# Kernel optimization log

Hardware: AMD Instinct MI355X
Metric: run time of the kernel (lower is better)

Reference implementation:

```python
import jax, jax.numpy as jnp
import numpy as np

A = 100000          # num atoms
E = 1600000         # num edges
N_SPECIES = 4       # len(atomic_types)
N_RADIAL = 8        # l=1 radial functions (max_radial hyper)
N_PSEUDO = 4        # Alchemical pseudo species
D = N_RADIAL * N_PSEUDO  # embedding_dim = 32
RC = 5.0            # cutoff radius
WIDTH = 0.5         # shifted-cosine width


def setup_inputs() -> dict:
    key = jax.random.key(0)
    ks = jax.random.split(key, 9)
    return {
        "interatomic_vectors": jax.random.normal(ks[0], (E, 3), dtype=jnp.float32),
        "centers": jax.random.randint(ks[1], (E,), 0, A),
        "neighbors": jax.random.randint(ks[2], (E,), 0, A),
        "species": jax.random.randint(ks[3], (A,), 0, N_SPECIES),
        "structures": jnp.sort(jax.random.randint(ks[4], (A,), 0, 64)),
        "atom_index_in_structure": jax.random.randint(ks[5], (A,), 0, A),
        # learned params
        "W_alch": jax.random.normal(ks[6], (N_SPECIES, N_PSEUDO), dtype=jnp.float32) * 0.1,
        "center_embedding": jax.random.normal(ks[7], (N_SPECIES, D), dtype=jnp.float32),
        "W_contract": jax.random.normal(ks[8], (3, D), dtype=jnp.float32) * (1.0 / np.sqrt(D)),
    }


def _shifted_cosine(d):
    # 1 below rc-width, smooth cosine taper to 0 at rc
    inner = RC - WIDTH
    taper = 0.5 * (jnp.cos(jnp.pi * (d - inner) / WIDTH) + 1.0)
    return jnp.where(d < inner, 1.0, jnp.where(d < RC, taper, 0.0))


def reference(interatomic_vectors, centers, neighbors, species, structures,
              atom_index_in_structure, W_alch, center_embedding, W_contract):
    eps = 1e-12
    d = jnp.sqrt(jnp.sum(interatomic_vectors * interatomic_vectors, axis=1) + eps)  # (E,)
    fc = _shifted_cosine(d)                                                         # (E,)
    # Laplacian-eigenstate-style l=1 radial basis: sin(n*pi*d/rc)/d, n=1..N_RADIAL
    n = jnp.arange(1, N_RADIAL + 1, dtype=jnp.float32)
    R = jnp.sin(n[None, :] * (jnp.pi / RC) * d[:, None]) / d[:, None]               # (E, nR)
    # real l=1 spherical harmonics, m order (-1, 0, 1) -> (y, z, x)/d
    Y = interatomic_vectors[:, jnp.array([1, 2, 0])] / d[:, None]                   # (E, 3)
    # alchemical pseudo-species weights of the neighbor
    alch = W_alch[species[neighbors]]                                               # (E, nQ)
    # per-edge expansion coefficients, scattered onto centers
    edge = (fc[:, None, None, None]
            * Y[:, :, None, None]
            * R[:, None, :, None]
            * alch[:, None, None, :])                                               # (E, 3, nR, nQ)
    spex = jax.ops.segment_sum(edge, centers, num_segments=A)                       # (A, 3, nR, nQ)
    x = spex.reshape(A, 3, D)                                                       # reshape(n,q -> n*q)
    x = x * center_embedding[species][:, None, :]                                   # center encoding
    out = jnp.einsum("amd,od->amo", x, W_contract)                                  # (A, 3, 3)
    return out
```

## Files before the change

kernel.cpp:

```cpp
#include <hip/hip_runtime.h>
#include <hip/hip_fp16.h>


constexpr int NSP  = 4;
constexpr int NRAD = 8;
constexpr int NPS  = 4;
constexpr int DDIM = NRAD * NPS;

constexpr int APB       = 128;
constexpr int APB_SH    = 7;
constexpr int NBIN_PAD  = 832;
constexpr int NROWS_PAD = 832;
constexpr int RS        = 840;
constexpr int PH1_BLK   = 512;
constexpr int PH1_U     = 4;
constexpr int PH1_REC   = PH1_BLK * PH1_U;
constexpr int CAP2      = 1536;
constexpr int IT2       = CAP2 / 256;

__device__ __forceinline__ unsigned pack2(float a, float b) {
    union { __half2 h; unsigned u; } cv;
    cv.h = __floats2half2_rn(a, b);
    return cv.u;
}
__device__ __forceinline__ float2 unpack2(unsigned u) {
    union { unsigned u; __half2 h; } cv;
    cv.u = u;
    return __half22float2(cv.h);
}

__device__ __forceinline__ void build_w2(
    float* sW2, const float* cemb, const float* Wc, const float* W_alch,
    int tid, int nthreads)
{
    for (int i = tid; i < 3 * NRAD * 16; i += nthreads) {
        int p  = i & 15;
        int n  = (i >> 4) & 7;
        int o  = i >> 7;
        int sc = p >> 2, sn = p & 3;
        float w = 0.0f;
        #pragma unroll
        for (int q = 0; q < NPS; q++)
            w += cemb[sc * DDIM + n * NPS + q] * Wc[o * DDIM + n * NPS + q]
               * W_alch[sn * NPS + q];
        sW2[i] = w;
    }
}

__device__ __forceinline__ bool edge_math(
    float vx, float vy, float vz, int pair, const float* sW2,
    float g[3], float t[3])
{
    float d2    = vx * vx + vy * vy + vz * vz + 1e-12f;
    float d     = sqrtf(d2);
    float inv_d = 1.0f / d;

    const float PI = 3.14159265358979323846f;
    const float RCUT = 5.0f, INNER = 4.5f, INVW = 2.0f;
    if (d >= RCUT) return false;
    float taper = 0.5f * (cosf(PI * (d - INNER) * INVW) + 1.0f);
    float fc = (d < INNER) ? 1.0f : taper;

    float theta = (PI / RCUT) * d;
    float s1 = sinf(theta);
    float c1 = cosf(theta);
    float two_c = 2.0f * c1;
    float R[NRAD];
    R[0] = s1 * inv_d;
    float sm2 = 0.0f, sm1 = s1;
    #pragma unroll
    for (int n = 1; n < NRAD; n++) {
        float s = two_c * sm1 - sm2;
        sm2 = sm1; sm1 = s;
        R[n] = s * inv_d;
    }

    #pragma unroll
    for (int o = 0; o < 3; o++) {
        float acc = 0.0f;
        #pragma unroll
        for (int n = 0; n < NRAD; n++)
            acc += R[n] * sW2[(o * NRAD + n) * 16 + pair];
        t[o] = acc;
    }
    g[0] = fc * vy * inv_d;
    g[1] = fc * vz * inv_d;
    g[2] = fc * vx * inv_d;
    return true;
}

__global__ __launch_bounds__(PH1_BLK) void vb_phase1(
    const float* __restrict__ vecs,
    const int*   __restrict__ centers,
    const int*   __restrict__ neighbors,
    const int*   __restrict__ species,
    const float* __restrict__ W_alch,
    const float* __restrict__ cemb,
    const float* __restrict__ Wc,
    unsigned short* __restrict__ runoff,
    int4*        __restrict__ payload,
    int E, int nbin)
{
    __shared__ float sW2[3 * NRAD * 16];
    __shared__ int4  srec[PH1_REC];
    __shared__ unsigned lcntP[NBIN_PAD / 2];
    __shared__ unsigned short lexcl[NBIN_PAD];
    __shared__ int sTotal;

    int tid = threadIdx.x;
    build_w2(sW2, cemb, Wc, W_alch, tid, PH1_BLK);
    for (int i = tid; i < NBIN_PAD / 2; i += PH1_BLK) lcntP[i] = 0;
    __syncthreads();

    int4 rec[PH1_U];
    int  rnk[PH1_U];
    #pragma unroll
    for (int u = 0; u < PH1_U; u++) {
        int e = blockIdx.x * PH1_REC + u * PH1_BLK + tid;
        rec[u].x = -1;
        rnk[u]   = 0;
        if (e < E) {
            float vx = vecs[3 * e + 0];
            float vy = vecs[3 * e + 1];
            float vz = vecs[3 * e + 2];
            int c  = centers[e];
            int pair = species[c] * 4 + species[neighbors[e]];
            float g[3], t[3];
            if (edge_math(vx, vy, vz, pair, sW2, g, t)) {
                rec[u].x = c;
                rec[u].y = (int)pack2(g[0], g[1]);
                rec[u].z = (int)pack2(g[2], t[0]);
                rec[u].w = (int)pack2(t[1], t[2]);
                int bin = c >> APB_SH;
                int sh  = (bin & 1) << 4;
                unsigned old = atomicAdd(&lcntP[bin >> 1], 1u << sh);
                rnk[u] = (int)((old >> sh) & 0xffff);
            }
        }
    }
    __syncthreads();

    if (tid < 64) {
        int base = tid * 13;
        int pre[13];
        int sum = 0;
        #pragma unroll
        for (int j = 0; j < 13; j++) {
            int b = base + j;
            int n = (lcntP[b >> 1] >> ((b & 1) << 4)) & 0xffff;
            pre[j] = sum; sum += n;
        }
        int incl = sum;
        #pragma unroll
        for (int off = 1; off < 64; off <<= 1) {
            int t = __shfl_up(incl, off, 64);
            if (tid >= off) incl += t;
        }
        int ex = incl - sum;
        #pragma unroll
        for (int j = 0; j < 13; j++)
            lexcl[base + j] = (unsigned short)(ex + pre[j]);
        if (tid == 63) sTotal = incl;
    }
    __syncthreads();

    #pragma unroll
    for (int u = 0; u < PH1_U; u++) {
        if (rec[u].x >= 0) {
            int bin = rec[u].x >> APB_SH;
            srec[(int)lexcl[bin] + rnk[u]] = rec[u];
        }
    }
    __syncthreads();

    int total = sTotal;
    size_t pbase = (size_t)blockIdx.x * PH1_REC;
    for (int i = tid; i < total; i += PH1_BLK)
        payload[pbase + i] = srec[i];
    unsigned short* ro = runoff + (size_t)blockIdx.x * RS;
    for (int b = tid; b <= nbin; b += PH1_BLK)
        ro[b] = (b < nbin) ? lexcl[b] : (unsigned short)total;
}

__global__ __launch_bounds__(256) void vb_phase2(
    const unsigned short* __restrict__ runoff,
    const int4*           __restrict__ payload,
    float*                __restrict__ out,
    int A, int nblocks)
{
    __shared__ int4 srec2[CAP2];
    __shared__ unsigned short sidx[CAP2];
    __shared__ unsigned short sst[NROWS_PAD];
    __shared__ unsigned short roff[NROWS_PAD + 64];
    __shared__ int cnt[APB], aexcl[APB];
    __shared__ float sout[APB * 9];
    __shared__ int sTotal;

    int b   = blockIdx.x;
    int tid = threadIdx.x;

    for (int r = tid; r < NROWS_PAD; r += 256) {
        unsigned short s0 = 0, len = 0;
        if (r < nblocks) {
            const unsigned short* row = runoff + (size_t)r * RS + b;
            s0  = row[0];
            len = (unsigned short)(row[1] - row[0]);
        }
        sst[r]  = s0;
        roff[r] = len;
    }
    __syncthreads();

    if (tid < 64) {
        int base = tid * 13;
        int pre[13];
        int sum = 0;
        #pragma unroll
        for (int j = 0; j < 13; j++) { pre[j] = sum; sum += roff[base + j]; }
        int incl = sum;
        #pragma unroll
        for (int off = 1; off < 64; off <<= 1) {
            int t = __shfl_up(incl, off, 64);
            if (tid >= off) incl += t;
        }
        int ex = incl - sum;
        #pragma unroll
        for (int j = 0; j < 13; j++)
            roff[base + j] = (unsigned short)(ex + pre[j]);
        if (tid == 63) sTotal = incl;
    }
    __syncthreads();
    if (tid == 0) roff[NROWS_PAD] = (unsigned short)sTotal;
    __syncthreads();

    int total = sTotal;
    float acc[9] = {0,0,0,0,0,0,0,0,0};
    int half = tid >> 7;
    int atom = tid & (APB - 1);

    for (int w0 = 0; w0 < total; w0 += CAP2) {
        int wend = min(w0 + CAP2, total);
        int nc = wend - w0;

        if (tid < APB) cnt[tid] = 0;
        __syncthreads();

        int key6[IT2], rnk6[IT2];
        #pragma unroll
        for (int it = 0; it < IT2; it++) {
            int i = it * 256 + tid;
            key6[it] = -1;
            rnk6[it] = 0;
            if (i < nc) {
                int p = w0 + i;
                int l = 0, h = nblocks;
                #pragma unroll 1
                while (h - l > 1) {
                    int m = (l + h) >> 1;
                    if ((int)roff[m] <= p) l = m; else h = m;
                }
                int j = p - (int)roff[l];
                int4 r = payload[(size_t)l * PH1_REC + (int)sst[l] + j];
                srec2[i] = r;
                int k = r.x & (APB - 1);
                key6[it] = k;
                rnk6[it] = atomicAdd(&cnt[k], 1);
            }
        }
        __syncthreads();

        if (tid < 64) {
            int c0 = cnt[2 * tid], c1 = cnt[2 * tid + 1];
            int s1 = c0 + c1;
            int incl = s1;
            #pragma unroll
            for (int off = 1; off < 64; off <<= 1) {
                int t = __shfl_up(incl, off, 64);
                if (tid >= off) incl += t;
            }
            int ex = incl - s1;
            aexcl[2 * tid]     = ex;
            aexcl[2 * tid + 1] = ex + c0;
        }
        __syncthreads();

        #pragma unroll
        for (int it = 0; it < IT2; it++) {
            if (key6[it] >= 0)
                sidx[aexcl[key6[it]] + rnk6[it]] =
                    (unsigned short)(it * 256 + tid);
        }
        __syncthreads();

        {
            int st = aexcl[atom], n = cnt[atom];
            int mid = st + ((n + 1) >> 1);
            int lo = half ? mid : st;
            int hi = half ? (st + n) : mid;
            for (int j = lo; j < hi; j++) {
                int4 r = srec2[sidx[j]];
                float2 g01 = unpack2((unsigned)r.y);
                float2 g2t = unpack2((unsigned)r.z);
                float2 t12 = unpack2((unsigned)r.w);
                float g0 = g01.x, g1 = g01.y, g2 = g2t.x;
                float t0 = g2t.y, t1 = t12.x, t2 = t12.y;
                acc[0] += g0 * t0; acc[1] += g0 * t1; acc[2] += g0 * t2;
                acc[3] += g1 * t0; acc[4] += g1 * t1; acc[5] += g1 * t2;
                acc[6] += g2 * t0; acc[7] += g2 * t1; acc[8] += g2 * t2;
            }
        }
        __syncthreads();
    }

    if (half == 0) {
        #pragma unroll
        for (int k = 0; k < 9; k++) sout[atom * 9 + k] = acc[k];
    }
    __syncthreads();
    if (half == 1) {
        #pragma unroll
        for (int k = 0; k < 9; k++) sout[atom * 9 + k] += acc[k];
    }
    __syncthreads();
    size_t gbase = (size_t)b * APB * 9;
    size_t lim = (size_t)A * 9;
    for (int i = tid; i < APB * 9; i += 256) {
        size_t gi = gbase + i;
        if (gi < lim) out[gi] = sout[i];
    }
}

__global__ __launch_bounds__(256) void vb_edge_fallback(
    const float* __restrict__ vecs,
    const int*   __restrict__ centers,
    const int*   __restrict__ neighbors,
    const int*   __restrict__ species,
    const float* __restrict__ W_alch,
    const float* __restrict__ cemb,
    const float* __restrict__ Wc,
    float*       __restrict__ out,
    int E)
{
    __shared__ float sW2[3 * NRAD * 16];
    build_w2(sW2, cemb, Wc, W_alch, threadIdx.x, blockDim.x);
    __syncthreads();

    int e = blockIdx.x * blockDim.x + threadIdx.x;
    if (e >= E) return;
    float vx = vecs[3 * e + 0], vy = vecs[3 * e + 1], vz = vecs[3 * e + 2];
    int c = centers[e];
    int pair = species[c] * 4 + species[neighbors[e]];
    float g[3], t[3];
    if (!edge_math(vx, vy, vz, pair, sW2, g, t)) return;
    float* op = out + (size_t)c * 9;
    #pragma unroll
    for (int m = 0; m < 3; m++)
        #pragma unroll
        for (int o = 0; o < 3; o++)
            atomicAdd(op + m * 3 + o, g[m] * t[o]);
}

extern "C" void kernel_launch(void* const* d_in, const int* in_sizes, int n_in,
                              void* d_out, int out_size, void* d_ws, size_t ws_size,
                              hipStream_t stream) {
    const float* vecs      = (const float*)d_in[0];
    const int*   centers   = (const int*)d_in[1];
    const int*   neighbors = (const int*)d_in[2];
    const int*   species   = (const int*)d_in[3];
    const float* W_alch    = (const float*)d_in[6];
    const float* cemb      = (const float*)d_in[7];
    const float* Wc        = (const float*)d_in[8];
    float*       out       = (float*)d_out;

    int E = in_sizes[1];
    int A = in_sizes[3];
    int nbin    = (A + APB - 1) >> APB_SH;
    int nblocks = (E + PH1_REC - 1) / PH1_REC;

    size_t ro_bytes = ((size_t)nblocks * RS * 2 + 255) & ~(size_t)255;
    size_t need = ro_bytes + (size_t)nblocks * PH1_REC * 16;

    if (nbin + 1 <= RS && nbin <= NBIN_PAD && nblocks <= NROWS_PAD &&
        need <= ws_size) {
        unsigned short* runoff = (unsigned short*)d_ws;
        int4* payload = (int4*)((char*)d_ws + ro_bytes);

        vb_phase1<<<nblocks, PH1_BLK, 0, stream>>>(vecs, centers, neighbors,
                                                   species, W_alch, cemb, Wc,
                                                   runoff, payload, E, nbin);
        vb_phase2<<<nbin, 256, 0, stream>>>(runoff, payload, out, A, nblocks);
    } else {
        hipMemsetAsync(d_out, 0, (size_t)out_size * sizeof(float), stream);
        int grid = (E + 255) / 256;
        vb_edge_fallback<<<grid, 256, 0, stream>>>(vecs, centers, neighbors,
                                                   species, W_alch, cemb, Wc,
                                                   out, E);
    }
}
```

Before: 129.2 us.

## Scatter records directly in phase2, pack counters, use fast trig intrinsics

Phase 2 now holds the fetched payload records in registers and writes them straight into their sorted positions in shared memory. This removes the separate index array and the indirect read during accumulation. Per-atom counters are packed two per 32-bit word using 16-bit atomics, the window capacity is enlarged, and the kernel gets a launch bound hint of 4 blocks. Edge math switches to the fast __sinf/__cosf intrinsics. The trade-offs are more register pressure from holding 7 int4 records per thread, and slightly lower trig accuracy.

```diff
diff --git a/kernel.cpp b/kernel.cpp
--- a/kernel.cpp
+++ b/kernel.cpp
@@ -15,7 +15,7 @@
 constexpr int PH1_BLK   = 512;
 constexpr int PH1_U     = 4;
 constexpr int PH1_REC   = PH1_BLK * PH1_U;
-constexpr int CAP2      = 1536;
+constexpr int CAP2      = 1792;
 constexpr int IT2       = CAP2 / 256;
 
 __device__ __forceinline__ unsigned pack2(float a, float b) {
@@ -58,12 +58,12 @@
     const float PI = 3.14159265358979323846f;
     const float RCUT = 5.0f, INNER = 4.5f, INVW = 2.0f;
     if (d >= RCUT) return false;
-    float taper = 0.5f * (cosf(PI * (d - INNER) * INVW) + 1.0f);
+    float taper = 0.5f * (__cosf(PI * (d - INNER) * INVW) + 1.0f);
     float fc = (d < INNER) ? 1.0f : taper;
 
     float theta = (PI / RCUT) * d;
-    float s1 = sinf(theta);
-    float c1 = cosf(theta);
+    float s1 = __sinf(theta);
+    float c1 = __cosf(theta);
     float two_c = 2.0f * c1;
     float R[NRAD];
     R[0] = s1 * inv_d;
@@ -182,17 +182,17 @@
         ro[b] = (b < nbin) ? lexcl[b] : (unsigned short)total;
 }
 
-__global__ __launch_bounds__(256) void vb_phase2(
+__global__ __launch_bounds__(256, 4) void vb_phase2(
     const unsigned short* __restrict__ runoff,
     const int4*           __restrict__ payload,
     float*                __restrict__ out,
     int A, int nblocks)
 {
     __shared__ int4 srec2[CAP2];
-    __shared__ unsigned short sidx[CAP2];
     __shared__ unsigned short sst[NROWS_PAD];
-    __shared__ unsigned short roff[NROWS_PAD + 64];
-    __shared__ int cnt[APB], aexcl[APB];
+    __shared__ unsigned short roff[NROWS_PAD];
+    __shared__ unsigned cntP[APB / 2];
+    __shared__ unsigned short aexcl[APB];
     __shared__ float sout[APB * 9];
     __shared__ int sTotal;
 
@@ -230,8 +230,6 @@
         if (tid == 63) sTotal = incl;
     }
     __syncthreads();
-    if (tid == 0) roff[NROWS_PAD] = (unsigned short)sTotal;
-    __syncthreads();
 
     int total = sTotal;
     float acc[9] = {0,0,0,0,0,0,0,0,0};
@@ -239,18 +237,17 @@
     int atom = tid & (APB - 1);
 
     for (int w0 = 0; w0 < total; w0 += CAP2) {
-        int wend = min(w0 + CAP2, total);
-        int nc = wend - w0;
-
-        if (tid < APB) cnt[tid] = 0;
+        int nc = min(CAP2, total - w0);
+
+        if (tid < APB / 2) cntP[tid] = 0;
         __syncthreads();
 
-        int key6[IT2], rnk6[IT2];
+        int4 rec[IT2];
+        int  krnk[IT2];
         #pragma unroll
         for (int it = 0; it < IT2; it++) {
             int i = it * 256 + tid;
-            key6[it] = -1;
-            rnk6[it] = 0;
+            krnk[it] = -1;
             if (i < nc) {
                 int p = w0 + i;
                 int l = 0, h = nblocks;
@@ -260,17 +257,19 @@
                     if ((int)roff[m] <= p) l = m; else h = m;
                 }
                 int j = p - (int)roff[l];
-                int4 r = payload[(size_t)l * PH1_REC + (int)sst[l] + j];
-                srec2[i] = r;
-                int k = r.x & (APB - 1);
-                key6[it] = k;
-                rnk6[it] = atomicAdd(&cnt[k], 1);
+                rec[it] = payload[(size_t)l * PH1_REC + (int)sst[l] + j];
+                int k = rec[it].x & (APB - 1);
+                int sh = (k & 1) << 4;
+                unsigned old = atomicAdd(&cntP[k >> 1], 1u << sh);
+                int rnk = (int)((old >> sh) & 0xffff);
+                krnk[it] = (rnk << 8) | k;
             }
         }
         __syncthreads();
 
         if (tid < 64) {
-            int c0 = cnt[2 * tid], c1 = cnt[2 * tid + 1];
+            unsigned cp = cntP[tid];
+            int c0 = (int)(cp & 0xffff), c1 = (int)(cp >> 16);
             int s1 = c0 + c1;
             int incl = s1;
             #pragma unroll
@@ -279,26 +278,29 @@
                 if (tid >= off) incl += t;
             }
             int ex = incl - s1;
-            aexcl[2 * tid]     = ex;
-            aexcl[2 * tid + 1] = ex + c0;
+            aexcl[2 * tid]     = (unsigned short)ex;
+            aexcl[2 * tid + 1] = (unsigned short)(ex + c0);
         }
         __syncthreads();
 
         #pragma unroll
         for (int it = 0; it < IT2; it++) {
-            if (key6[it] >= 0)
-                sidx[aexcl[key6[it]] + rnk6[it]] =
-                    (unsigned short)(it * 256 + tid);
+            if (krnk[it] >= 0) {
+                int k = krnk[it] & (APB - 1);
+                srec2[(int)aexcl[k] + (krnk[it] >> 8)] = rec[it];
+            }
         }
         __syncthreads();
 
         {
-            int st = aexcl[atom], n = cnt[atom];
+            int st = (int)aexcl[atom];
+            unsigned cp = cntP[atom >> 1];
+            int n = (int)((cp >> ((atom & 1) << 4)) & 0xffff);
             int mid = st + ((n + 1) >> 1);
             int lo = half ? mid : st;
             int hi = half ? (st + n) : mid;
             for (int j = lo; j < hi; j++) {
-                int4 r = srec2[sidx[j]];
+                int4 r = srec2[j];
                 float2 g01 = unpack2((unsigned)r.y);
                 float2 g2t = unpack2((unsigned)r.z);
                 float2 t12 = unpack2((unsigned)r.w);
@@ -380,7 +382,7 @@
     size_t ro_bytes = ((size_t)nblocks * RS * 2 + 255) & ~(size_t)255;
     size_t need = ro_bytes + (size_t)nblocks * PH1_REC * 16;
 
-    if (nbin + 1 <= RS && nbin <= NBIN_PAD && nblocks <= NROWS_PAD &&
+    if (nbin + 1 <= RS && nbin <= NBIN_PAD && nblocks < NROWS_PAD &&
         need <= ws_size) {
         unsigned short* runoff = (unsigned short*)d_ws;
         int4* payload = (int4*)((char*)d_ws + ro_bytes);
```

After: 157.8 us. 22.1% more time.
